# Performance work log

Hardware: AMD Instinct MI355X
Metric: run time of the kernel (lower is better)

Reference implementation:

```python
import jax, jax.numpy as jnp
import numpy as np

DIM = 2048
NH = 16      # query heads
NKV = 4      # kv heads
HD = 128     # head dim
NREP = NH // NKV
B = 2
T = 2048
NEG = -1e30  # masked-score value (safe for softmax grads)


def setup_inputs() -> dict:
    key = jax.random.key(0)
    ks = jax.random.split(key, 5)
    x = jax.random.normal(ks[0], (B, T, DIM), jnp.float32)
    # nn.Linear(in, out, bias=False) -> stored here as [in, out] for x @ W
    wq = jax.random.normal(ks[1], (DIM, NH * HD), jnp.float32) * 0.02
    wk = jax.random.normal(ks[2], (DIM, NKV * HD), jnp.float32) * 0.02
    wv = jax.random.normal(ks[3], (DIM, NKV * HD), jnp.float32) * 0.02
    wo = jax.random.normal(ks[4], (NH * HD, DIM), jnp.float32) * 0.02
    # standard RoPE freqs: complex freqs_cis stored as (cos, sin) pairs [T, HD//2, 2]
    inv_freq = 1.0 / (10000.0 ** (np.arange(0, HD, 2, dtype=np.float64) / HD))
    angles = np.outer(np.arange(T, dtype=np.float64), inv_freq)
    freqs_cis = jnp.asarray(np.stack([np.cos(angles), np.sin(angles)], axis=-1),
                            dtype=jnp.float32)
    return {"x": x, "wq": wq, "wk": wk, "wv": wv, "wo": wo, "freqs_cis": freqs_cis}


def _rope(t, cos, sin):
    # t: [B,H,T,HD]; cos/sin broadcast to [1,1,T,HD//2]
    tr = t.reshape(t.shape[:-1] + (HD // 2, 2))
    t0, t1 = tr[..., 0], tr[..., 1]  # real/imag of complex pairs
    return jnp.stack([t0 * cos - t1 * sin, t0 * sin + t1 * cos], axis=-1).reshape(t.shape)


def reference(x, wq, wk, wv, wo, freqs_cis):
    # QKV projections
    q = (x @ wq).reshape(B, T, NH, HD).transpose(0, 2, 1, 3)    # [B,NH,T,HD]
    k = (x @ wk).reshape(B, T, NKV, HD).transpose(0, 2, 1, 3)   # [B,NKV,T,HD]
    v = (x @ wv).reshape(B, T, NKV, HD).transpose(0, 2, 1, 3)
    cos = freqs_cis[..., 0][None, None]  # [1,1,T,HD//2]
    sin = freqs_cis[..., 1][None, None]
    q = _rope(q, cos, sin)
    k = _rope(k, cos, sin)
    new_cache_k, new_cache_v = k, v
    # GQA attention without materializing repeat_interleave: group queries per kv head
    qg = q.reshape(B, NKV, NREP, T, HD)
    scale = 1.0 / jnp.sqrt(jnp.float32(HD))
    scores = jnp.einsum('bgrtd,bgsd->bgrts', qg, k) * scale      # [B,NKV,NREP,T,T]
    causal = jnp.tril(jnp.ones((T, T), dtype=bool))
    scores = jnp.where(causal, scores, NEG)
    attn = jax.nn.softmax(scores, axis=-1)
    out = jnp.einsum('bgrts,bgsd->bgrtd', attn, v)               # [B,NKV,NREP,T,HD]
    out = out.reshape(B, NH, T, HD).transpose(0, 2, 1, 3).reshape(B, T, NH * HD)
    return out @ wo, new_cache_k, new_cache_v
```

## Files before the change

### kernel.cpp

```cpp
#include <hip/hip_runtime.h>
#include <hip/hip_bf16.h>

#define DIM 2048
#define NH 16
#define NKV 4
#define HD 128
#define B_ 2
#define T_ 2048
#define M_TOT (B_*T_)
#define NQKV 3072

typedef __attribute__((ext_vector_type(8))) short short8;
typedef __attribute__((ext_vector_type(4))) short short4_t;
typedef __attribute__((ext_vector_type(4))) float f32x4;

typedef const __attribute__((address_space(1))) void* gptr_t;
typedef __attribute__((address_space(3))) void* lptr_t;

__device__ __forceinline__ ushort f2bf(float f) {
  unsigned u = __builtin_bit_cast(unsigned, f);
  u += 0x7fffu + ((u >> 16) & 1u);
  return (ushort)(u >> 16);
}

__global__ __launch_bounds__(256) void prep_kernel(
    const float* __restrict__ x, const float* __restrict__ wq,
    const float* __restrict__ wk, const float* __restrict__ wv,
    const float* __restrict__ wo,
    ushort* __restrict__ x_bf, ushort* __restrict__ wqkv_t, ushort* __restrict__ wo_t) {
  __shared__ float tile[32][33];
  int id = blockIdx.x, tid = threadIdx.x;
  if (id < 4096) {
    int i = id*256 + tid;
    const float4* p = (const float4*)x + (size_t)i*2;
    float4 a = p[0], b = p[1];
    short8 o;
    o[0]=f2bf(a.x); o[1]=f2bf(a.y); o[2]=f2bf(a.z); o[3]=f2bf(a.w);
    o[4]=f2bf(b.x); o[5]=f2bf(b.y); o[6]=f2bf(b.z); o[7]=f2bf(b.w);
    *((short8*)x_bf + i) = o;
    return;
  }
  const float* in; ushort* out; int lg, tt;
  if (id < 8192)       { in = wq; out = wqkv_t;                    lg = 6; tt = id - 4096; }
  else if (id < 9216)  { in = wk; out = wqkv_t + (size_t)2048*DIM; lg = 4; tt = id - 8192; }
  else if (id < 10240) { in = wv; out = wqkv_t + (size_t)2560*DIM; lg = 4; tt = id - 9216; }
  else                 { in = wo; out = wo_t;                      lg = 6; tt = id - 10240; }
  int N = 32 << lg;
  int n0 = (tt & ((1 << lg) - 1))*32, k0 = (tt >> lg)*32;
  int tx = tid & 31, ty = tid >> 5;
  #pragma unroll
  for (int i=0;i<32;i+=8) tile[ty+i][tx] = in[(size_t)(k0+ty+i)*N + n0+tx];
  __syncthreads();
  #pragma unroll
  for (int i=0;i<32;i+=8) out[(size_t)(n0+ty+i)*DIM + k0+tx] = f2bf(tile[tx][ty+i]);
}

__global__ __launch_bounds__(256) void gemm_bt(const ushort* __restrict__ A, const ushort* __restrict__ Bt,
                                               float* __restrict__ C, int M, int N, int K) {
  __shared__ ushort Ash[128*64];
  __shared__ ushort Bsh[128*64];
  int tid = threadIdx.x;
  int lane = tid & 63, wave = tid >> 6;
  int lo = lane & 15, hi = lane >> 4;
  int m0 = blockIdx.y * 128, n0 = blockIdx.x * 128;
  int wr = wave >> 1, wc = wave & 1;
  f32x4 acc[4][4] = {};
  int srow = tid >> 3;
  int scol = (tid & 7) * 8;
  const ushort* Abase = A + (size_t)(m0 + srow)*K + scol;
  const ushort* Bbase = Bt + (size_t)(n0 + srow)*K + scol;
  for (int k0 = 0; k0 < K; k0 += 64) {
    #pragma unroll
    for (int c = 0; c < 4; ++c)
      __builtin_amdgcn_global_load_lds((gptr_t)(Abase + (size_t)c*32*K + k0),
                                       (lptr_t)&Ash[(srow + c*32)*64 + scol], 16, 0, 0);
    #pragma unroll
    for (int c = 0; c < 4; ++c)
      __builtin_amdgcn_global_load_lds((gptr_t)(Bbase + (size_t)c*32*K + k0),
                                       (lptr_t)&Bsh[(srow + c*32)*64 + scol], 16, 0, 0);
    __syncthreads();
    #pragma unroll
    for (int kk = 0; kk < 2; ++kk) {
      short8 a[4], b[4];
      #pragma unroll
      for (int m=0;m<4;m++) a[m] = *(const short8*)&Ash[(wr*64 + m*16 + lo)*64 + kk*32 + hi*8];
      #pragma unroll
      for (int n=0;n<4;n++) b[n] = *(const short8*)&Bsh[(wc*64 + n*16 + lo)*64 + kk*32 + hi*8];
      #pragma unroll
      for (int m=0;m<4;m++)
        #pragma unroll
        for (int n=0;n<4;n++)
          acc[m][n] = __builtin_amdgcn_mfma_f32_16x16x32_bf16(a[m], b[n], acc[m][n], 0, 0, 0);
    }
    __syncthreads();
  }
  #pragma unroll
  for (int m=0;m<4;m++)
    #pragma unroll
    for (int n=0;n<4;n++) {
      int row = m0 + wr*64 + m*16 + hi*4;
      int col = n0 + wc*64 + n*16 + lo;
      #pragma unroll
      for (int r=0;r<4;r++)
        C[(size_t)(row + r)*N + col] = acc[m][n][r];
    }
}

__global__ __launch_bounds__(256) void gemm_qkv_rope(
    const ushort* __restrict__ A, const ushort* __restrict__ Bt,
    const float* __restrict__ freqs,
    ushort* __restrict__ q_bf, ushort* __restrict__ k_bf,
    float* __restrict__ kcache, float* __restrict__ vcache,
    ushort* __restrict__ v_t) {
  const int K = DIM;
  __shared__ ushort Ash[128*64];
  __shared__ ushort Bsh[128*64];
  int tid = threadIdx.x;
  int lane = tid & 63, wave = tid >> 6;
  int lo = lane & 15, hi = lane >> 4;
  int m0 = blockIdx.y * 128, n0 = blockIdx.x * 128;
  int wr = wave >> 1, wc = wave & 1;
  f32x4 acc[4][4] = {};
  int srow = tid >> 3;
  int scol = (tid & 7) * 8;
  const ushort* Abase = A + (size_t)(m0 + srow)*K + scol;
  const ushort* Bbase = Bt + (size_t)(n0 + srow)*K + scol;
  for (int k0 = 0; k0 < K; k0 += 64) {
    #pragma unroll
    for (int c = 0; c < 4; ++c)
      __builtin_amdgcn_global_load_lds((gptr_t)(Abase + (size_t)c*32*K + k0),
                                       (lptr_t)&Ash[(srow + c*32)*64 + scol], 16, 0, 0);
    #pragma unroll
    for (int c = 0; c < 4; ++c)
      __builtin_amdgcn_global_load_lds((gptr_t)(Bbase + (size_t)c*32*K + k0),
                                       (lptr_t)&Bsh[(srow + c*32)*64 + scol], 16, 0, 0);
    __syncthreads();
    #pragma unroll
    for (int kk = 0; kk < 2; ++kk) {
      short8 a[4], b[4];
      #pragma unroll
      for (int m=0;m<4;m++) a[m] = *(const short8*)&Ash[(wr*64 + m*16 + lo)*64 + kk*32 + hi*8];
      #pragma unroll
      for (int n=0;n<4;n++) b[n] = *(const short8*)&Bsh[(wc*64 + n*16 + lo)*64 + kk*32 + hi*8];
      #pragma unroll
      for (int m=0;m<4;m++)
        #pragma unroll
        for (int n=0;n<4;n++)
          acc[m][n] = __builtin_amdgcn_mfma_f32_16x16x32_bf16(a[m], b[n], acc[m][n], 0, 0, 0);
    }
    __syncthreads();
  }
  const float QSCALE = 0.08838834764831845f * 1.4426950408889634f;
  #pragma unroll
  for (int m=0;m<4;m++) {
    int row0 = m0 + wr*64 + m*16 + hi*4;
    int bb = row0 >> 11, t0 = row0 & 2047;
    #pragma unroll
    for (int n=0;n<4;n++) {
      int col = n0 + wc*64 + n*16 + lo;
      f32x4 a = acc[m][n];
      if (col < 2048) {
        int hh = col >> 7, d = col & 127, jj = d >> 1;
        bool ev = (d & 1) == 0;
        #pragma unroll
        for (int r=0;r<4;r++) {
          float p = __shfl_xor(a[r], 1);
          float2 cs = ((const float2*)freqs)[(size_t)(t0 + r)*64 + jj];
          float o = ev ? (a[r]*cs.x - p*cs.y) : (a[r]*cs.x + p*cs.y);
          q_bf[((size_t)(bb*NH + hh)*T_ + t0 + r)*HD + d] = f2bf(o * QSCALE);
        }
      } else if (col < 2560) {
        int cg = col - 2048;
        int gg = cg >> 7, d = cg & 127, jj = d >> 1;
        bool ev = (d & 1) == 0;
        #pragma unroll
        for (int r=0;r<4;r++) {
          float p = __shfl_xor(a[r], 1);
          float2 cs = ((const float2*)freqs)[(size_t)(t0 + r)*64 + jj];
          float o = ev ? (a[r]*cs.x - p*cs.y) : (a[r]*cs.x + p*cs.y);
          size_t idx = ((size_t)(bb*NKV + gg)*T_ + t0 + r)*HD + d;
          k_bf[idx] = f2bf(o);
          kcache[idx] = o;
        }
      } else {
        int cg = col - 2560;
        int gg = cg >> 7, d = cg & 127;
        short4_t pk;
        #pragma unroll
        for (int r=0;r<4;r++) {
          vcache[((size_t)(bb*NKV + gg)*T_ + t0 + r)*HD + d] = a[r];
          pk[r] = (short)f2bf(a[r]);
        }
        *(short4_t*)&v_t[((size_t)(bb*NKV + gg)*HD + d)*T_ + t0] = pk;
      }
    }
  }
}

__global__ __launch_bounds__(256) void attn_kernel(const ushort* __restrict__ Qb, const ushort* __restrict__ Kb,
                          const ushort* __restrict__ Vt, ushort* __restrict__ O) {
  __shared__ ushort Ksh[128][144];
  __shared__ unsigned Pshu[4][16][40];
  int id = blockIdx.x;
  int j = id >> 5, hb = id & 31;
  int t2 = j >> 3, u = j & 7;
  int qt = (t2==0) ? u : (t2==1) ? 15-u : (t2==2) ? 16+u : 31-u;
  int h = hb & 15, b = hb >> 4, g = h >> 2;
  int tid = threadIdx.x, wave = tid >> 6, lane = tid & 63;
  int lo = lane & 15, hi = lane >> 4;
  int q0 = qt*64 + wave*16;
  const ushort* Qrow = Qb + ((size_t)(b*NH + h)*T_ + q0 + lo)*HD;
  short8 qfr[4];
  #pragma unroll
  for (int kf=0;kf<4;kf++) qfr[kf] = *(const short8*)(Qrow + kf*32 + hi*8);
  f32x4 o[8] = {};
  float m_run = -1e30f, l_run = 0.f;
  const ushort* Kbase = Kb + (size_t)(b*NKV + g)*T_*HD;
  const ushort* Vbase = Vt + (size_t)(b*NKV + g)*HD*T_;
  int ntiles = (qt >> 1) + 1;
  for (int it = 0; it < ntiles; ++it) {
    int kv0 = it*128;
    {
      int r = tid >> 4, cl = (tid & 15)*8;
      #pragma unroll
      for (int c=0;c<8;c++)
        *(short8*)&Ksh[r + c*16][cl] = *(const short8*)(Kbase + (size_t)(kv0 + r + c*16)*HD + cl);
    }
    __syncthreads();
    f32x4 s[8];
    __builtin_amdgcn_s_setprio(1);
    #pragma unroll
    for (int nf=0;nf<8;nf++) {
      s[nf] = (f32x4){0.f,0.f,0.f,0.f};
      #pragma unroll
      for (int kf=0;kf<4;kf++) {
        short8 bk = *(const short8*)&Ksh[nf*16 + lo][kf*32 + hi*8];
        s[nf] = __builtin_amdgcn_mfma_f32_16x16x32_bf16(bk, qfr[kf], s[nf], 0,0,0);
      }
    }
    __builtin_amdgcn_s_setprio(0);
    if (it == ntiles-1) {
      int qg = q0 + lo;
      #pragma unroll
      for (int nf=0;nf<8;nf++)
        #pragma unroll
        for (int r=0;r<4;r++) {
          int kvg = kv0 + nf*16 + hi*4 + r;
          if (kvg > qg) s[nf][r] = -1e30f;
        }
    }
    float mx = -1e30f;
    #pragma unroll
    for (int nf=0;nf<8;nf++)
      #pragma unroll
      for (int r=0;r<4;r++) mx = fmaxf(mx, s[nf][r]);
    mx = fmaxf(mx, __shfl_xor(mx, 16));
    mx = fmaxf(mx, __shfl_xor(mx, 32));
    float nm = fmaxf(m_run, mx);
    float scl = exp2f(m_run - nm);
    m_run = nm;
    float rs = 0.f;
    #pragma unroll
    for (int nf=0;nf<8;nf++)
      #pragma unroll
      for (int r=0;r<4;r++) { float pv = exp2f(s[nf][r] - nm); s[nf][r] = pv; rs += pv; }
    rs += __shfl_xor(rs, 16);
    rs += __shfl_xor(rs, 32);
    l_run = l_run*scl + rs;
    float ps[4];
    #pragma unroll
    for (int r=0;r<4;r++) ps[r] = __shfl(scl, (lane & 48) + hi*4 + r);
    #pragma unroll
    for (int df=0;df<8;df++)
      #pragma unroll
      for (int r=0;r<4;r++) o[df][r] *= ps[r];
    #pragma unroll
    for (int h2=0; h2<2; ++h2) {
      #pragma unroll
      for (int nf4=0;nf4<4;nf4++) {
        f32x4 sv = s[h2*4 + nf4];
        Pshu[wave][lo][nf4*8 + hi*2]     = (unsigned)f2bf(sv[0]) | ((unsigned)f2bf(sv[1]) << 16);
        Pshu[wave][lo][nf4*8 + hi*2 + 1] = (unsigned)f2bf(sv[2]) | ((unsigned)f2bf(sv[3]) << 16);
      }
      asm volatile("s_waitcnt lgkmcnt(0)" ::: "memory");
      short8 pa[2];
      #pragma unroll
      for (int k2=0;k2<2;k2++)
        pa[k2] = *(const short8*)&((const ushort*)&Pshu[wave][lo][0])[k2*32 + hi*8];
      __builtin_amdgcn_s_setprio(1);
      #pragma unroll
      for (int df=0;df<8;df++) {
        #pragma unroll
        for (int k2=0;k2<2;k2++) {
          short8 bv = *(const short8*)(Vbase + (size_t)(df*16 + lo)*T_ + kv0 + h2*64 + k2*32 + hi*8);
          o[df] = __builtin_amdgcn_mfma_f32_16x16x32_bf16(pa[k2], bv, o[df], 0,0,0);
        }
      }
      __builtin_amdgcn_s_setprio(0);
    }
    __syncthreads();
  }
  #pragma unroll
  for (int r=0;r<4;r++) {
    float li = __shfl(l_run, (lane & 48) + hi*4 + r);
    float inv = 1.0f / li;
    int qg = q0 + hi*4 + r;
    size_t base = ((size_t)(b*T_) + qg)*DIM + (size_t)h*HD;
    #pragma unroll
    for (int df=0;df<8;df++)
      O[base + df*16 + lo] = f2bf(o[df][r] * inv);
  }
}

extern "C" void kernel_launch(void* const* d_in, const int* in_sizes, int n_in,
                              void* d_out, int out_size, void* d_ws, size_t ws_size,
                              hipStream_t stream) {
  const float* x     = (const float*)d_in[0];
  const float* wq    = (const float*)d_in[1];
  const float* wk    = (const float*)d_in[2];
  const float* wv    = (const float*)d_in[3];
  const float* wo    = (const float*)d_in[4];
  const float* freqs = (const float*)d_in[5];
  float* out    = (float*)d_out;
  float* kcache = out + (size_t)B_*T_*DIM;
  float* vcache = kcache + (size_t)B_*NKV*T_*HD;

  char* ws = (char*)d_ws;
  size_t off = 0;
  auto alloc = [&](size_t bytes) { char* p = ws + off; off += (bytes + 255) & ~255ULL; return p; };
  ushort* x_bf   = (ushort*)alloc((size_t)M_TOT*DIM*2);
  ushort* wqkv_t = (ushort*)alloc((size_t)NQKV*DIM*2);
  ushort* wo_t   = (ushort*)alloc((size_t)DIM*DIM*2);
  ushort* q_bf   = (ushort*)alloc((size_t)B_*NH*T_*HD*2);
  ushort* k_bf   = (ushort*)alloc((size_t)B_*NKV*T_*HD*2);
  ushort* v_t    = (ushort*)alloc((size_t)B_*NKV*HD*T_*2);
  ushort* ao_bf  = (ushort*)alloc((size_t)M_TOT*DIM*2);
  (void)ws_size; (void)in_sizes; (void)n_in; (void)out_size;

  prep_kernel<<<14336, 256, 0, stream>>>(x, wq, wk, wv, wo, x_bf, wqkv_t, wo_t);

  gemm_qkv_rope<<<dim3(NQKV/128, M_TOT/128), 256, 0, stream>>>(
      x_bf, wqkv_t, freqs, q_bf, k_bf, kcache, vcache, v_t);

  attn_kernel<<<1024, 256, 0, stream>>>(q_bf, k_bf, v_t, ao_bf);

  gemm_bt<<<dim3(DIM/128, M_TOT/128), 256, 0, stream>>>(ao_bf, wo_t, out, M_TOT, DIM, DIM);
}
```

Measured before the change: 431.0 us.

## Double-buffer K tiles in LDS with register prefetch and lazy softmax rescale

The attention kernel now walks 64-key tiles instead of 128 and double-buffers K in shared memory. The next tile is prefetched into registers while the current tile's QK^T and PV MFMAs run, then stored into the alternate buffer, which leaves one barrier per iteration instead of a load-sync-compute chain. It also skips the online-softmax rescale of the output accumulator unless the running max grows by more than 8 (log2 domain), and uses raw v_exp_f32 and v_cvt_pk_bf16_f32 in place of exp2f and manual rounding. In exchange it runs twice as many iterations with smaller MFMA batches, and the thresholded rescale and fast exp slightly change numerics (possible overflow headroom risk).

Result: faster. 417.8 us (-3.1%).

```diff
diff --git a/kernel.cpp b/kernel.cpp
--- a/kernel.cpp
+++ b/kernel.cpp
@@ -21,6 +21,18 @@
   unsigned u = __builtin_bit_cast(unsigned, f);
   u += 0x7fffu + ((u >> 16) & 1u);
   return (ushort)(u >> 16);
+}
+
+__device__ __forceinline__ float fast_exp2(float x) {
+  float r;
+  asm("v_exp_f32 %0, %1" : "=v"(r) : "v"(x));
+  return r;
+}
+
+__device__ __forceinline__ unsigned cvt_pk_bf16(float a, float b) {
+  unsigned r;
+  asm("v_cvt_pk_bf16_f32 %0, %1, %2" : "=v"(r) : "v"(a), "v"(b));
+  return r;
 }
 
 __global__ __launch_bounds__(256) void prep_kernel(
@@ -199,7 +211,7 @@
 
 __global__ __launch_bounds__(256) void attn_kernel(const ushort* __restrict__ Qb, const ushort* __restrict__ Kb,
                           const ushort* __restrict__ Vt, ushort* __restrict__ O) {
-  __shared__ ushort Ksh[128][144];
+  __shared__ ushort Ksh[2][64][144];
   __shared__ unsigned Pshu[4][16][40];
   int id = blockIdx.x;
   int j = id >> 5, hb = id & 31;
@@ -217,24 +229,30 @@
   float m_run = -1e30f, l_run = 0.f;
   const ushort* Kbase = Kb + (size_t)(b*NKV + g)*T_*HD;
   const ushort* Vbase = Vt + (size_t)(b*NKV + g)*HD*T_;
-  int ntiles = (qt >> 1) + 1;
+  int ntiles = qt + 1;
+  int sr = tid >> 4, scl8 = (tid & 15)*8;
+  #pragma unroll
+  for (int c=0;c<4;c++)
+    *(short8*)&Ksh[0][sr + c*16][scl8] = *(const short8*)(Kbase + (size_t)(sr + c*16)*HD + scl8);
+  __syncthreads();
+  int cur = 0;
   for (int it = 0; it < ntiles; ++it) {
-    int kv0 = it*128;
-    {
-      int r = tid >> 4, cl = (tid & 15)*8;
-      #pragma unroll
-      for (int c=0;c<8;c++)
-        *(short8*)&Ksh[r + c*16][cl] = *(const short8*)(Kbase + (size_t)(kv0 + r + c*16)*HD + cl);
-    }
-    __syncthreads();
-    f32x4 s[8];
+    int kv0 = it*64;
+    short8 kreg[4];
+    bool pre = (it+1 < ntiles);
+    if (pre) {
+      #pragma unroll
+      for (int c=0;c<4;c++)
+        kreg[c] = *(const short8*)(Kbase + (size_t)(kv0 + 64 + sr + c*16)*HD + scl8);
+    }
+    f32x4 s[4];
     __builtin_amdgcn_s_setprio(1);
     #pragma unroll
-    for (int nf=0;nf<8;nf++) {
+    for (int nf=0;nf<4;nf++) {
       s[nf] = (f32x4){0.f,0.f,0.f,0.f};
       #pragma unroll
       for (int kf=0;kf<4;kf++) {
-        short8 bk = *(const short8*)&Ksh[nf*16 + lo][kf*32 + hi*8];
+        short8 bk = *(const short8*)&Ksh[cur][nf*16 + lo][kf*32 + hi*8];
         s[nf] = __builtin_amdgcn_mfma_f32_16x16x32_bf16(bk, qfr[kf], s[nf], 0,0,0);
       }
     }
@@ -242,7 +260,7 @@
     if (it == ntiles-1) {
       int qg = q0 + lo;
       #pragma unroll
-      for (int nf=0;nf<8;nf++)
+      for (int nf=0;nf<4;nf++)
         #pragma unroll
         for (int r=0;r<4;r++) {
           int kvg = kv0 + nf*16 + hi*4 + r;
@@ -251,54 +269,59 @@
     }
     float mx = -1e30f;
     #pragma unroll
-    for (int nf=0;nf<8;nf++)
+    for (int nf=0;nf<4;nf++)
       #pragma unroll
       for (int r=0;r<4;r++) mx = fmaxf(mx, s[nf][r]);
     mx = fmaxf(mx, __shfl_xor(mx, 16));
     mx = fmaxf(mx, __shfl_xor(mx, 32));
-    float nm = fmaxf(m_run, mx);
-    float scl = exp2f(m_run - nm);
-    m_run = nm;
+    if (!__all(mx - m_run <= 8.0f)) {
+      float nm = fmaxf(m_run, mx);
+      float scl = fast_exp2(m_run - nm);
+      float ps[4];
+      #pragma unroll
+      for (int r=0;r<4;r++) ps[r] = __shfl(scl, (lane & 48) + hi*4 + r);
+      #pragma unroll
+      for (int df=0;df<8;df++)
+        #pragma unroll
+        for (int r=0;r<4;r++) o[df][r] *= ps[r];
+      l_run *= scl;
+      m_run = nm;
+    }
     float rs = 0.f;
     #pragma unroll
-    for (int nf=0;nf<8;nf++)
-      #pragma unroll
-      for (int r=0;r<4;r++) { float pv = exp2f(s[nf][r] - nm); s[nf][r] = pv; rs += pv; }
+    for (int nf=0;nf<4;nf++)
+      #pragma unroll
+      for (int r=0;r<4;r++) { float pv = fast_exp2(s[nf][r] - m_run); s[nf][r] = pv; rs += pv; }
     rs += __shfl_xor(rs, 16);
     rs += __shfl_xor(rs, 32);
-    l_run = l_run*scl + rs;
-    float ps[4];
-    #pragma unroll
-    for (int r=0;r<4;r++) ps[r] = __shfl(scl, (lane & 48) + hi*4 + r);
-    #pragma unroll
-    for (int df=0;df<8;df++)
-      #pragma unroll
-      for (int r=0;r<4;r++) o[df][r] *= ps[r];
-    #pragma unroll
-    for (int h2=0; h2<2; ++h2) {
-      #pragma unroll
-      for (int nf4=0;nf4<4;nf4++) {
-        f32x4 sv = s[h2*4 + nf4];
-        Pshu[wave][lo][nf4*8 + hi*2]     = (unsigned)f2bf(sv[0]) | ((unsigned)f2bf(sv[1]) << 16);
-        Pshu[wave][lo][nf4*8 + hi*2 + 1] = (unsigned)f2bf(sv[2]) | ((unsigned)f2bf(sv[3]) << 16);
+    l_run += rs;
+    #pragma unroll
+    for (int nf=0;nf<4;nf++) {
+      Pshu[wave][lo][nf*8 + hi*2]     = cvt_pk_bf16(s[nf][0], s[nf][1]);
+      Pshu[wave][lo][nf*8 + hi*2 + 1] = cvt_pk_bf16(s[nf][2], s[nf][3]);
+    }
+    asm volatile("s_waitcnt lgkmcnt(0)" ::: "memory");
+    short8 pa[2];
+    #pragma unroll
+    for (int k2=0;k2<2;k2++)
+      pa[k2] = *(const short8*)&((const ushort*)&Pshu[wave][lo][0])[k2*32 + hi*8];
+    __builtin_amdgcn_s_setprio(1);
+    #pragma unroll
+    for (int df=0;df<8;df++) {
+      #pragma unroll
+      for (int k2=0;k2<2;k2++) {
+        short8 bv = *(const short8*)(Vbase + (size_t)(df*16 + lo)*T_ + kv0 + k2*32 + hi*8);
+        o[df] = __builtin_amdgcn_mfma_f32_16x16x32_bf16(pa[k2], bv, o[df], 0,0,0);
       }
-      asm volatile("s_waitcnt lgkmcnt(0)" ::: "memory");
-      short8 pa[2];
-      #pragma unroll
-      for (int k2=0;k2<2;k2++)
-        pa[k2] = *(const short8*)&((const ushort*)&Pshu[wave][lo][0])[k2*32 + hi*8];
-      __builtin_amdgcn_s_setprio(1);
-      #pragma unroll
-      for (int df=0;df<8;df++) {
-        #pragma unroll
-        for (int k2=0;k2<2;k2++) {
-          short8 bv = *(const short8*)(Vbase + (size_t)(df*16 + lo)*T_ + kv0 + h2*64 + k2*32 + hi*8);
-          o[df] = __builtin_amdgcn_mfma_f32_16x16x32_bf16(pa[k2], bv, o[df], 0,0,0);
-        }
-      }
-      __builtin_amdgcn_s_setprio(0);
-    }
-    __syncthreads();
+    }
+    __builtin_amdgcn_s_setprio(0);
+    if (pre) {
+      #pragma unroll
+      for (int c=0;c<4;c++)
+        *(short8*)&Ksh[cur^1][sr + c*16][scl8] = kreg[c];
+    }
+    __syncthreads();
+    cur ^= 1;
   }
   #pragma unroll
   for (int r=0;r<4;r++) {
```
